# Performance work log

Hardware: AMD Instinct MI355X
Metric: run time of the kernel (lower is better)

Reference implementation:

```python
import jax, jax.numpy as jnp
import numpy as np

B, T, D, NH, F = 8, 1024, 1152, 16, 4304
HD = D // NH


def _ln(x, w, b, eps=1e-5):
    m = jnp.mean(x, axis=-1, keepdims=True)
    v = jnp.mean((x - m) ** 2, axis=-1, keepdims=True)
    return (x - m) * jax.lax.rsqrt(v + eps) * w + b


def setup_inputs() -> dict:
    key = jax.random.key(0)
    ks = jax.random.split(key, 8)
    s = 0.02
    return {
        "x": jax.random.normal(ks[0], (B, T, D), jnp.float32),
        "ln1_w": jnp.ones((D,), jnp.float32),
        "ln1_b": jnp.zeros((D,), jnp.float32),
        "wq": jax.random.normal(ks[1], (D, D), jnp.float32) * s,
        "bq": jnp.zeros((D,), jnp.float32),
        "wk": jax.random.normal(ks[2], (D, D), jnp.float32) * s,
        "bk": jnp.zeros((D,), jnp.float32),
        "wv": jax.random.normal(ks[3], (D, D), jnp.float32) * s,
        "bv": jnp.zeros((D,), jnp.float32),
        "wo": jax.random.normal(ks[4], (D, D), jnp.float32) * s,
        "bo": jnp.zeros((D,), jnp.float32),
        "ln2_w": jnp.ones((D,), jnp.float32),
        "ln2_b": jnp.zeros((D,), jnp.float32),
        "w1": jax.random.normal(ks[5], (F, D), jnp.float32) * s,
        "b1": jnp.zeros((F,), jnp.float32),
        "w2": jax.random.normal(ks[6], (D, F), jnp.float32) * s,
        "b2": jnp.zeros((D,), jnp.float32),
    }


def reference(x, ln1_w, ln1_b, wq, bq, wk, bk, wv, bv, wo, bo,
              ln2_w, ln2_b, w1, b1, w2, b2):
    b, t, d = x.shape
    h = _ln(x, ln1_w, ln1_b)
    q = h @ wq.T + bq
    k = h @ wk.T + bk
    v = h @ wv.T + bv
    # Faithful to torch: .view(B, H, T, hd) with NO transpose (non-standard split)
    q = q.reshape(b, NH, t, HD)
    k = k.reshape(b, NH, t, HD)
    v = v.reshape(b, NH, t, HD)
    scale = HD ** -0.5
    att = jnp.einsum('bhtd,bhsd->bhts', q, k) * scale  # [B,H,T,T]
    scores = jax.nn.softmax(att, axis=-1)  # dropout skipped (eval mode)
    o = jnp.einsum('bhts,bhsd->bhtd', scores, v)
    o = o.transpose(0, 2, 1, 3).reshape(b, t, d)  # transpose(1,2) + flatten(2)
    o = o @ wo.T + bo
    x1 = o + x
    h2 = _ln(x1, ln2_w, ln2_b)
    f = jax.nn.gelu(h2 @ w1.T + b1, approximate=True)
    return f @ w2.T + b2 + x1
```

## Files before the change

### kernel.cpp

```cpp
#include <hip/hip_runtime.h>
#include <cstddef>
#include <cstdint>


constexpr int kB = 8, kT = 1024, kD = 1152, kNH = 16, kF = 4304, kHD = 72;
constexpr int kNT = kB * kT;
constexpr int kFP = 4352;
constexpr int kEP = 96;
constexpr int kEV = 80;
constexpr int kFC = 2176;

typedef short bf16x8 __attribute__((ext_vector_type(8)));
typedef float f32x4 __attribute__((ext_vector_type(4)));

__device__ __forceinline__ ushort f2bf(float f) {
  union { float f; uint u; } a; a.f = f;
  const uint r = a.u + 0x7FFFu + ((a.u >> 16) & 1u);
  return (ushort)(r >> 16);
}
__device__ __forceinline__ float gelu_tanh(float x) {
  const float u = 0.7978845608028654f * (x + 0.044715f * x * x * x);
  return 0.5f * x * (1.0f + tanhf(u));
}
#define GLL16(g, s) __builtin_amdgcn_global_load_lds( \
    (const __attribute__((address_space(1))) void*)(g), \
    (__attribute__((address_space(3))) void*)(s), 16, 0, 0)

__global__ __launch_bounds__(256) void ln_kernel(const float* __restrict__ in,
                                                 const float* __restrict__ w,
                                                 const float* __restrict__ b,
                                                 ushort* __restrict__ out) {
  const int row = blockIdx.x;
  const float4* r4 = reinterpret_cast<const float4*>(in + (size_t)row * kD);
  const float4* w4 = reinterpret_cast<const float4*>(w);
  const float4* b4 = reinterpret_cast<const float4*>(b);
  const int t = threadIdx.x;
  float4 v0 = r4[t];
  float4 v1 = make_float4(0.f, 0.f, 0.f, 0.f);
  const bool second = (t < kD / 4 - 256);
  if (second) v1 = r4[t + 256];
  float s  = v0.x + v0.y + v0.z + v0.w + v1.x + v1.y + v1.z + v1.w;
  float ss = v0.x * v0.x + v0.y * v0.y + v0.z * v0.z + v0.w * v0.w +
             v1.x * v1.x + v1.y * v1.y + v1.z * v1.z + v1.w * v1.w;
  #pragma unroll
  for (int m = 1; m <= 32; m <<= 1) { s += __shfl_xor(s, m); ss += __shfl_xor(ss, m); }
  __shared__ float red[8];
  const int wave = t >> 6;
  if ((t & 63) == 0) { red[wave] = s; red[4 + wave] = ss; }
  __syncthreads();
  s  = red[0] + red[1] + red[2] + red[3];
  ss = red[4] + red[5] + red[6] + red[7];
  const float mean = s * (1.0f / kD);
  const float var  = ss * (1.0f / kD) - mean * mean;
  const float rs   = rsqrtf(var + 1e-5f);
  ushort4* o4 = reinterpret_cast<ushort4*>(out + (size_t)row * kD);
  {
    float4 W = w4[t], Bv = b4[t];
    ushort4 r;
    r.x = f2bf((v0.x - mean) * rs * W.x + Bv.x);
    r.y = f2bf((v0.y - mean) * rs * W.y + Bv.y);
    r.z = f2bf((v0.z - mean) * rs * W.z + Bv.z);
    r.w = f2bf((v0.w - mean) * rs * W.w + Bv.w);
    o4[t] = r;
  }
  if (second) {
    float4 W = w4[t + 256], Bv = b4[t + 256];
    ushort4 r;
    r.x = f2bf((v1.x - mean) * rs * W.x + Bv.x);
    r.y = f2bf((v1.y - mean) * rs * W.y + Bv.y);
    r.z = f2bf((v1.z - mean) * rs * W.z + Bv.z);
    r.w = f2bf((v1.w - mean) * rs * W.w + Bv.w);
    o4[t + 256] = r;
  }
}

__global__ __launch_bounds__(256) void cvt4_kernel(const float* __restrict__ src,
                                                   ushort* __restrict__ dst, int n4) {
  const int i = blockIdx.x * 256 + threadIdx.x;
  if (i < n4) {
    const float4 v = reinterpret_cast<const float4*>(src)[i];
    ushort4 r = { f2bf(v.x), f2bf(v.y), f2bf(v.z), f2bf(v.w) };
    reinterpret_cast<ushort4*>(dst)[i] = r;
  }
}
__global__ __launch_bounds__(256) void cvtw2_kernel(const float* __restrict__ src,
                                                    ushort* __restrict__ dst) {
  const int i = blockIdx.x * 256 + threadIdx.x;
  if (i >= kD * (kFP / 4)) return;
  const int r = i / (kFP / 4), c4 = i % (kFP / 4);
  const int c = c4 * 4;
  ushort4 o;
  if (c < kF) {
    const float4 v = *reinterpret_cast<const float4*>(src + (size_t)r * kF + c);
    o = { f2bf(v.x), f2bf(v.y), f2bf(v.z), f2bf(v.w) };
  } else o = { 0, 0, 0, 0 };
  reinterpret_cast<ushort4*>(dst + (size_t)r * kFP)[c4] = o;
}
__global__ __launch_bounds__(256) void b1pad_kernel(const float* __restrict__ src,
                                                    float* __restrict__ dst,
                                                    ushort* __restrict__ w1b) {
  const int i = blockIdx.x * 256 + threadIdx.x;
  if (i < kFP) dst[i] = (i < kF) ? src[i] : 0.f;
  const int j = i - kFP;
  if (j >= 0 && j < (kFP - kF) * kD) w1b[(size_t)kF * kD + j] = 0;
}
__global__ __launch_bounds__(256) void zfill_kernel(ushort* __restrict__ kp,
                                                    ushort* __restrict__ vt) {
  const int i = blockIdx.x * 256 + threadIdx.x;
  const int nk = 131072 * 24;
  if (i < nk) {
    const int row = i / 24, c = 72 + i % 24;
    kp[(size_t)row * kEP + c] = 0;
  } else {
    const int j = i - nk;
    if (j < 131072 * 8) {
      const int bh = j >> 13, rem = j & 8191;
      const int e = 72 + (rem >> 10), s = rem & 1023;
      vt[((size_t)bh * kEV + e) * 1024 + s] = 0;
    }
  }
}

template <int MODE, int GELU_, int BIAS_, int RES_>
__global__ __launch_bounds__(256) void gemm_mfma(
    const ushort* __restrict__ A, const ushort* __restrict__ W,
    const float* __restrict__ bias, const float* __restrict__ bias2,
    const float* __restrict__ bias3, const float* __restrict__ res,
    void* __restrict__ Cout, void* __restrict__ C2, void* __restrict__ C3,
    int M, int K, int ldw) {
  __shared__ __align__(16) ushort As[128 * 32];
  __shared__ __align__(16) ushort Bs[128 * 32];
  const int tid = threadIdx.x;
  const int l = tid & 63, w = tid >> 6;
  const int lr = l & 15, lg = l >> 4;
  const int wm = w >> 1, wn = w & 1;
  const int bn = blockIdx.x, bm = blockIdx.y;
  f32x4 acc[4][4] = {};
  const int srow = 32 * w + (l >> 2);
  const int scol = (l & 3) << 3;
  const ushort* Ag = A + (size_t)(bn * 128 + srow) * K + scol;
  const ushort* Wg = W + (size_t)(bm * 128 + srow) * ldw + scol;
  for (int k0 = 0; k0 < K; k0 += 32) {
    __syncthreads();
    #pragma unroll
    for (int i = 0; i < 2; i++) {
      GLL16(Ag + (size_t)(16 * i) * K + k0, &As[(32 * w + 16 * i) * 32]);
      GLL16(Wg + (size_t)(16 * i) * ldw + k0, &Bs[(32 * w + 16 * i) * 32]);
    }
    __syncthreads();
    bf16x8 af[4], bf[4];
    #pragma unroll
    for (int mf = 0; mf < 4; mf++)
      af[mf] = *(const bf16x8*)&As[(wm * 64 + mf * 16 + lr) * 32 + lg * 8];
    #pragma unroll
    for (int nf = 0; nf < 4; nf++)
      bf[nf] = *(const bf16x8*)&Bs[(wn * 64 + nf * 16 + lr) * 32 + lg * 8];
    #pragma unroll
    for (int mf = 0; mf < 4; mf++)
      #pragma unroll
      for (int nf = 0; nf < 4; nf++)
        acc[mf][nf] = __builtin_amdgcn_mfma_f32_16x16x32_bf16(af[mf], bf[nf], acc[mf][nf], 0, 0, 0);
  }
  if (MODE == 4) {
    const int proj = bm / 9;
    const float* bp = proj == 0 ? bias : (proj == 1 ? bias2 : bias3);
    ushort* dstp = (ushort*)(proj == 0 ? Cout : (proj == 1 ? C2 : C3));
    #pragma unroll
    for (int mf = 0; mf < 4; mf++) {
      #pragma unroll
      for (int nf = 0; nf < 4; nf++) {
        const int c = bm * 128 + wn * 64 + nf * 16 + lr;
        const int cl = c - proj * kD;
        const int jj = cl / 72, e = cl - jj * 72;
        const float bv = bp[cl];
        #pragma unroll
        for (int j = 0; j < 4; j++) {
          const int r = bn * 128 + wm * 64 + mf * 16 + lg * 4 + j;
          float v = acc[mf][nf][j] + bv;
          if (proj == 0) v *= 0.11785113019775793f;
          const int b = r >> 10, t = r & 1023;
          const int h = t >> 6, u = t & 63;
          const int s = u * 16 + jj, bh = b * 16 + h;
          const size_t dst = (proj < 2) ? ((size_t)bh * 1024 + s) * kEP + e
                                        : ((size_t)bh * kEV + e) * 1024 + s;
          dstp[dst] = f2bf(v);
        }
      }
    }
    return;
  }
  #pragma unroll
  for (int mf = 0; mf < 4; mf++) {
    #pragma unroll
    for (int nf = 0; nf < 4; nf++) {
      const int c = bm * 128 + wn * 64 + nf * 16 + lr;
      const float bv = BIAS_ ? bias[c] : 0.f;
      #pragma unroll
      for (int j = 0; j < 4; j++) {
        const int r = bn * 128 + wm * 64 + mf * 16 + lg * 4 + j;
        float v = acc[mf][nf][j] + bv;
        if (GELU_) v = gelu_tanh(v);
        if (RES_) v += res[(size_t)r * M + c];
        if (MODE == 0) ((float*)Cout)[(size_t)r * M + c] = v;
        else           ((ushort*)Cout)[(size_t)r * M + c] = f2bf(v);
      }
    }
  }
}

__global__ __launch_bounds__(256, 2) void attn_kernel(
    const ushort* __restrict__ qp, const ushort* __restrict__ kp,
    const ushort* __restrict__ vt, ushort* __restrict__ ob) {
  __shared__ __align__(16) ushort Kt[64 * 96];
  __shared__ __align__(16) ushort Vt[80 * 64];
  const int tid = threadIdx.x, l = tid & 63, w = tid >> 6;
  const int lr = l & 15, lg = l >> 4;
  const int qb = blockIdx.x, hh = blockIdx.y, bb = blockIdx.z;
  const int bh = bb * 16 + hh;
  const int s0 = qb * 256 + w * 64;
  bf16x8 qf[4][3];
  const ushort* qbase = qp + (size_t)bh * 1024 * kEP;
  #pragma unroll
  for (int qi = 0; qi < 4; qi++)
    #pragma unroll
    for (int ks = 0; ks < 3; ks++)
      qf[qi][ks] = *(const bf16x8*)(qbase + (size_t)(s0 + qi * 16 + lr) * kEP + ks * 32 + lg * 8);
  float mstate[4], lstate[4];
  #pragma unroll
  for (int i = 0; i < 4; i++) { mstate[i] = -1e30f; lstate[i] = 0.f; }
  f32x4 oacc[4][5] = {};
  const ushort* ktile0 = kp + (size_t)bh * 1024 * kEP;
  const ushort* vbase  = vt + (size_t)bh * kEV * 1024;
  const int srcA = lr + 32 * (lg & 1);
  const int srcB = srcA + 16;
  const int hi = lg >> 1;
  const int rmap = (lg << 4) + (lg << 2);

  for (int kt = 0; kt < 16; kt++) {
    __syncthreads();
    {
      const ushort* kg = ktile0 + (size_t)kt * 64 * kEP;
      #pragma unroll
      for (int i = 0; i < 3; i++) {
        const int is = w * 3 + i;
        GLL16(kg + is * 512 + l * 8, &Kt[is * 512]);
      }
    }
    {
      #pragma unroll
      for (int i = 0; i < 3; i++) {
        const int is = w + i * 4;
        if (is < 10) {
          const int e = is * 8 + (l >> 3);
          const int cg = (l & 7) ^ (e & 7);
          GLL16(vbase + (size_t)e * 1024 + kt * 64 + cg * 8, &Vt[is * 512]);
        }
      }
    }
    __syncthreads();
    f32x4 sacc[4][4];
    #pragma unroll
    for (int si = 0; si < 4; si++)
      #pragma unroll
      for (int qi = 0; qi < 4; qi++)
        sacc[si][qi] = (f32x4){0.f, 0.f, 0.f, 0.f};
    #pragma unroll
    for (int ks = 0; ks < 3; ks++) {
      bf16x8 kf[4];
      #pragma unroll
      for (int si = 0; si < 4; si++)
        kf[si] = *(const bf16x8*)&Kt[(si * 16 + lr) * 96 + ks * 32 + lg * 8];
      #pragma unroll
      for (int si = 0; si < 4; si++)
        #pragma unroll
        for (int qi = 0; qi < 4; qi++)
          sacc[si][qi] = __builtin_amdgcn_mfma_f32_16x16x32_bf16(kf[si], qf[qi][ks], sacc[si][qi], 0, 0, 0);
    }
    #pragma unroll
    for (int qi = 0; qi < 4; qi++) {
      float mx = sacc[0][qi][0];
      #pragma unroll
      for (int si = 0; si < 4; si++)
        #pragma unroll
        for (int j = 0; j < 4; j++) mx = fmaxf(mx, sacc[si][qi][j]);
      mx = fmaxf(mx, __shfl_xor(mx, 16));
      mx = fmaxf(mx, __shfl_xor(mx, 32));
      const float mo = mstate[qi], mn = fmaxf(mo, mx);
      float sum = 0.f;
      #pragma unroll
      for (int si = 0; si < 4; si++)
        #pragma unroll
        for (int j = 0; j < 4; j++) {
          const float p = __expf(sacc[si][qi][j] - mn);
          sacc[si][qi][j] = p;
          sum += p;
        }
      sum += __shfl_xor(sum, 16);
      sum += __shfl_xor(sum, 32);
      const float al = __expf(mo - mn);
      lstate[qi] = lstate[qi] * al + sum;
      mstate[qi] = mn;
      #pragma unroll
      for (int j = 0; j < 4; j++) {
        const float alj = __shfl(al, rmap + j);
        #pragma unroll
        for (int ei = 0; ei < 5; ei++) oacc[qi][ei][j] *= alj;
      }
      uint wlo[4], whi[4];
      #pragma unroll
      for (int si = 0; si < 4; si++) {
        wlo[si] = (uint)f2bf(sacc[si][qi][0]) | ((uint)f2bf(sacc[si][qi][1]) << 16);
        whi[si] = (uint)f2bf(sacc[si][qi][2]) | ((uint)f2bf(sacc[si][qi][3]) << 16);
      }
      uint A0[4], A1[4], A2[4], A3[4];
      #pragma unroll
      for (int si = 0; si < 4; si++) {
        A0[si] = (uint)__shfl((int)wlo[si], srcA);
        A1[si] = (uint)__shfl((int)whi[si], srcA);
        A2[si] = (uint)__shfl((int)wlo[si], srcB);
        A3[si] = (uint)__shfl((int)whi[si], srcB);
      }
      union U { uint u[4]; bf16x8 v; } p0, p1;
      p0.u[0] = hi ? A0[1] : A0[0];  p0.u[1] = hi ? A1[1] : A1[0];
      p0.u[2] = hi ? A2[1] : A2[0];  p0.u[3] = hi ? A3[1] : A3[0];
      p1.u[0] = hi ? A0[3] : A0[2];  p1.u[1] = hi ? A1[3] : A1[2];
      p1.u[2] = hi ? A2[3] : A2[2];  p1.u[3] = hi ? A3[3] : A3[2];
      #pragma unroll
      for (int ei = 0; ei < 5; ei++) {
        const int e = ei * 16 + lr;
        const int sw = e & 7;
        bf16x8 vb0 = *(const bf16x8*)&Vt[e * 64 + ((0 + lg) ^ sw) * 8];
        bf16x8 vb1 = *(const bf16x8*)&Vt[e * 64 + ((4 + lg) ^ sw) * 8];
        oacc[qi][ei] = __builtin_amdgcn_mfma_f32_16x16x32_bf16(p0.v, vb0, oacc[qi][ei], 0, 0, 0);
        oacc[qi][ei] = __builtin_amdgcn_mfma_f32_16x16x32_bf16(p1.v, vb1, oacc[qi][ei], 0, 0, 0);
      }
    }
  }
  #pragma unroll
  for (int qi = 0; qi < 4; qi++) {
    const float rli = 1.f / lstate[qi];
    float lij[4];
    #pragma unroll
    for (int j = 0; j < 4; j++) lij[j] = __shfl(rli, rmap + j);
    #pragma unroll
    for (int ei = 0; ei < 5; ei++) {
      const int e = ei * 16 + lr;
      if (e < 72) {
        #pragma unroll
        for (int j = 0; j < 4; j++) {
          const int s = s0 + qi * 16 + lg * 4 + j;
          ob[((size_t)bb * 1024 + s) * kD + hh * kHD + e] =
              f2bf(oacc[qi][ei][j] * lij[j]);
        }
      }
    }
  }
}

extern "C" void kernel_launch(void* const* d_in, const int* in_sizes, int n_in,
                              void* d_out, int out_size, void* d_ws, size_t ws_size,
                              hipStream_t stream) {
  const float* x    = (const float*)d_in[0];
  const float* ln1w = (const float*)d_in[1];
  const float* ln1b = (const float*)d_in[2];
  const float* wq   = (const float*)d_in[3];
  const float* bq   = (const float*)d_in[4];
  const float* wk   = (const float*)d_in[5];
  const float* bk   = (const float*)d_in[6];
  const float* wv   = (const float*)d_in[7];
  const float* bv   = (const float*)d_in[8];
  const float* wo   = (const float*)d_in[9];
  const float* bo   = (const float*)d_in[10];
  const float* ln2w = (const float*)d_in[11];
  const float* ln2b = (const float*)d_in[12];
  const float* w1   = (const float*)d_in[13];
  const float* b1   = (const float*)d_in[14];
  const float* w2   = (const float*)d_in[15];
  const float* b2   = (const float*)d_in[16];
  float* out = (float*)d_out;

  ushort* ws = (ushort*)d_ws;
  const size_t nD = (size_t)kNT * kD;
  const size_t nQK = (size_t)kB * kNH * 1024 * kEP;
  const size_t nVT = (size_t)kB * kNH * kEV * 1024;
  ushort* hb  = ws;
  ushort* qp  = hb + nD;
  ushort* kp  = qp + nQK;
  ushort* vt  = kp + nQK;
  ushort* wqb = vt + nVT;
  ushort* wkb = wqb + (size_t)kD * kD;
  ushort* wvb = wkb + (size_t)kD * kD;
  ushort* wob = wvb + (size_t)kD * kD;
  ushort* w1b = wob + (size_t)kD * kD;
  ushort* w2b = w1b + (size_t)kFP * kD;
  float*  x1  = (float*)(w2b + (size_t)kD * kFP);
  float*  b1b = x1 + nD;
  ushort* ob  = hb;
  ushort* h2b = qp;
  ushort* fb  = kp;

  const dim3 blk(256);
  const dim3 gqkv(64, 27);
  const dim3 go(64, 9);
  const dim3 gm1(64, 17);
  const dim3 ga(4, 16, 8);

  const int nDD4 = kD * kD / 4;
  cvt4_kernel<<<(nDD4 + 255) / 256, blk, 0, stream>>>(wq, wqb, nDD4);
  cvt4_kernel<<<(nDD4 + 255) / 256, blk, 0, stream>>>(wk, wkb, nDD4);
  cvt4_kernel<<<(nDD4 + 255) / 256, blk, 0, stream>>>(wv, wvb, nDD4);
  cvt4_kernel<<<(nDD4 + 255) / 256, blk, 0, stream>>>(wo, wob, nDD4);
  const int nW14 = kF * kD / 4;
  cvt4_kernel<<<(nW14 + 255) / 256, blk, 0, stream>>>(w1, w1b, nW14);
  cvtw2_kernel<<<(kD * (kFP / 4) + 255) / 256, blk, 0, stream>>>(w2, w2b);
  b1pad_kernel<<<(kFP + (kFP - kF) * kD + 255) / 256, blk, 0, stream>>>(b1, b1b, w1b);
  zfill_kernel<<<16384, blk, 0, stream>>>(kp, vt);

  ln_kernel<<<kNT, blk, 0, stream>>>(x, ln1w, ln1b, hb);
  gemm_mfma<4, 0, 1, 0><<<gqkv, blk, 0, stream>>>(hb, wqb, bq, bk, bv, nullptr,
                                                  qp, kp, vt, kD, kD, kD);
  attn_kernel<<<ga, blk, 0, stream>>>(qp, kp, vt, ob);
  gemm_mfma<0, 0, 1, 1><<<go, blk, 0, stream>>>(ob, wob, bo, nullptr, nullptr, x,
                                                x1, nullptr, nullptr, kD, kD, kD);
  ln_kernel<<<kNT, blk, 0, stream>>>(x1, ln2w, ln2b, h2b);
  gemm_mfma<1, 1, 1, 0><<<gm1, blk, 0, stream>>>(h2b, w1b, b1b, nullptr, nullptr, nullptr,
                                                 fb, nullptr, nullptr, kFC, kD, kD);
  gemm_mfma<0, 0, 1, 1><<<go, blk, 0, stream>>>(fb, w2b, b2, nullptr, nullptr, x1,
                                                out, nullptr, nullptr, kD, kFC, kFP);
  gemm_mfma<1, 1, 1, 0><<<gm1, blk, 0, stream>>>(h2b, w1b + (size_t)kFC * kD, b1b + kFC,
                                                 nullptr, nullptr, nullptr,
                                                 fb, nullptr, nullptr, kFC, kD, kD);
  gemm_mfma<0, 0, 0, 1><<<go, blk, 0, stream>>>(fb, w2b + kFC, nullptr, nullptr, nullptr,
                                                out, out, nullptr, nullptr, kD, kFC, kFP);
}
```

Before: 873.6 us.

## Replace GEMMs with 256x256-tile double-buffered MFMA kernel and unsplit FFN

Replaces the 128x128 single-buffered GEMM with a 512-thread, 256x256-tile kernel. It double-buffers LDS, loads two k-stages ahead with a swizzled layout, and raises wave priority around the MFMA block. The FFN up- and down-projections are no longer split into two halves, because the whole GELU activation now fits in the reused q/k/v workspace. The larger tiles raise data reuse and hide load latency. The cost is more LDS and registers per block, out-of-range padded tiles that read past the weights and are masked at store time, and fewer blocks for the small GEMMs.

```diff
diff --git a/kernel.cpp b/kernel.cpp
--- a/kernel.cpp
+++ b/kernel.cpp
@@ -8,7 +8,6 @@
 constexpr int kFP = 4352;
 constexpr int kEP = 96;
 constexpr int kEV = 80;
-constexpr int kFC = 2176;
 
 typedef short bf16x8 __attribute__((ext_vector_type(8)));
 typedef float f32x4 __attribute__((ext_vector_type(4)));
@@ -121,88 +120,137 @@
   }
 }
 
-template <int MODE, int GELU_, int BIAS_, int RES_>
-__global__ __launch_bounds__(256) void gemm_mfma(
+template <int MODE, int GELU_>
+__global__ __launch_bounds__(512, 2) void gemm256(
     const ushort* __restrict__ A, const ushort* __restrict__ W,
     const float* __restrict__ bias, const float* __restrict__ bias2,
     const float* __restrict__ bias3, const float* __restrict__ res,
     void* __restrict__ Cout, void* __restrict__ C2, void* __restrict__ C3,
-    int M, int K, int ldw) {
-  __shared__ __align__(16) ushort As[128 * 32];
-  __shared__ __align__(16) ushort Bs[128 * 32];
+    int Mstride, int Mreal, int K, int ldw) {
+  __shared__ __align__(16) ushort Ab[2][256 * 32];
+  __shared__ __align__(16) ushort Bb[2][256 * 32];
   const int tid = threadIdx.x;
   const int l = tid & 63, w = tid >> 6;
   const int lr = l & 15, lg = l >> 4;
-  const int wm = w >> 1, wn = w & 1;
+  const int wm = w >> 2, wn = w & 3;
   const int bn = blockIdx.x, bm = blockIdx.y;
-  f32x4 acc[4][4] = {};
-  const int srow = 32 * w + (l >> 2);
-  const int scol = (l & 3) << 3;
-  const ushort* Ag = A + (size_t)(bn * 128 + srow) * K + scol;
-  const ushort* Wg = W + (size_t)(bm * 128 + srow) * ldw + scol;
-  for (int k0 = 0; k0 < K; k0 += 32) {
-    __syncthreads();
-    #pragma unroll
-    for (int i = 0; i < 2; i++) {
-      GLL16(Ag + (size_t)(16 * i) * K + k0, &As[(32 * w + 16 * i) * 32]);
-      GLL16(Wg + (size_t)(16 * i) * ldw + k0, &Bs[(32 * w + 16 * i) * 32]);
-    }
-    __syncthreads();
-    bf16x8 af[4], bf[4];
-    #pragma unroll
-    for (int mf = 0; mf < 4; mf++)
-      af[mf] = *(const bf16x8*)&As[(wm * 64 + mf * 16 + lr) * 32 + lg * 8];
-    #pragma unroll
-    for (int nf = 0; nf < 4; nf++)
-      bf[nf] = *(const bf16x8*)&Bs[(wn * 64 + nf * 16 + lr) * 32 + lg * 8];
-    #pragma unroll
-    for (int mf = 0; mf < 4; mf++)
-      #pragma unroll
-      for (int nf = 0; nf < 4; nf++)
-        acc[mf][nf] = __builtin_amdgcn_mfma_f32_16x16x32_bf16(af[mf], bf[nf], acc[mf][nf], 0, 0, 0);
-  }
+  const int NS = K >> 5;
+
+  const int r0 = tid >> 2, c0 = (tid & 3) ^ (r0 & 3);
+  const int r1 = (512 + tid) >> 2, c1 = (tid & 3) ^ (r1 & 3);
+  const ushort* Ag0 = A + (size_t)(bn * 256 + r0) * K + c0 * 8;
+  const ushort* Ag1 = A + (size_t)(bn * 256 + r1) * K + c1 * 8;
+  const ushort* Wg0 = W + (size_t)(bm * 256 + r0) * ldw + c0 * 8;
+  const ushort* Wg1 = W + (size_t)(bm * 256 + r1) * ldw + c1 * 8;
+  const int dst0 = (w * 64) * 8;
+  const int dst1 = (512 + w * 64) * 8;
+
+  const int swz = (lg ^ (lr & 3)) * 8;
+  const int abase = (wm * 128 + lr) * 32 + swz;
+  const int bbase = (wn * 64 + lr) * 32 + swz;
+
+  f32x4 acc[8][4] = {};
+  bf16x8 A0[8], A1[8], Bf[4];
+
+  GLL16(Ag0, &Ab[0][dst0]); GLL16(Ag1, &Ab[0][dst1]);
+  GLL16(Wg0, &Bb[0][dst0]); GLL16(Wg1, &Bb[0][dst1]);
+  GLL16(Ag0 + 32, &Ab[1][dst0]); GLL16(Ag1 + 32, &Ab[1][dst1]);
+  GLL16(Wg0 + 32, &Bb[1][dst0]); GLL16(Wg1 + 32, &Bb[1][dst1]);
+  asm volatile("s_waitcnt vmcnt(4)" ::: "memory");
+  __builtin_amdgcn_s_barrier();
+  #pragma unroll
+  for (int mf = 0; mf < 8; mf++)
+    A0[mf] = *(const bf16x8*)&Ab[0][abase + mf * 512];
+  asm volatile("s_waitcnt lgkmcnt(0)" ::: "memory");
+  __builtin_amdgcn_sched_barrier(0);
+
+#define GBODY(S, AC, AA)                                                      \
+  {                                                                           \
+    asm volatile("s_waitcnt vmcnt(0)" ::: "memory");  \
+    __builtin_amdgcn_s_barrier();                                             \
+    const ushort* bb_ = &Bb[(S) & 1][0];                                      \
+    _Pragma("unroll")                                                         \
+    for (int nf = 0; nf < 4; nf++)                                            \
+      Bf[nf] = *(const bf16x8*)&bb_[bbase + nf * 512];                        \
+    __builtin_amdgcn_sched_barrier(0);        \
+    if ((S) + 1 < NS) {                                                       \
+      const ushort* ab_ = &Ab[((S) + 1) & 1][0];                              \
+      _Pragma("unroll")                                                       \
+      for (int mf = 0; mf < 8; mf++)                                          \
+        AA[mf] = *(const bf16x8*)&ab_[abase + mf * 512];                      \
+    }                                                                         \
+    asm volatile("s_waitcnt lgkmcnt(8)" ::: "memory");     \
+    __builtin_amdgcn_sched_barrier(0);                                        \
+    if ((S) + 2 < NS) {                        \
+      const int k0_ = ((S) + 2) * 32;                                         \
+      GLL16(Ag0 + k0_, &Ab[(S) & 1][dst0]);                                   \
+      GLL16(Ag1 + k0_, &Ab[(S) & 1][dst1]);                                   \
+      GLL16(Wg0 + k0_, &Bb[(S) & 1][dst0]);                                   \
+      GLL16(Wg1 + k0_, &Bb[(S) & 1][dst1]);                                   \
+    }                                                                         \
+    __builtin_amdgcn_s_setprio(1);                                            \
+    _Pragma("unroll")                                                         \
+    for (int mf = 0; mf < 8; mf++)                                            \
+      _Pragma("unroll")                                                       \
+      for (int nf = 0; nf < 4; nf++)                                          \
+        acc[mf][nf] = __builtin_amdgcn_mfma_f32_16x16x32_bf16(                \
+            AC[mf], Bf[nf], acc[mf][nf], 0, 0, 0);                            \
+    __builtin_amdgcn_s_setprio(0);                                            \
+    asm volatile("s_waitcnt lgkmcnt(0)" ::: "memory");   \
+    __builtin_amdgcn_sched_barrier(0);                                        \
+  }
+
+  for (int t = 0; t < NS / 2; t++) {
+    GBODY(2 * t, A0, A1)
+    GBODY(2 * t + 1, A1, A0)
+  }
+#undef GBODY
+
   if (MODE == 4) {
-    const int proj = bm / 9;
-    const float* bp = proj == 0 ? bias : (proj == 1 ? bias2 : bias3);
-    ushort* dstp = (ushort*)(proj == 0 ? Cout : (proj == 1 ? C2 : C3));
-    #pragma unroll
-    for (int mf = 0; mf < 4; mf++) {
-      #pragma unroll
-      for (int nf = 0; nf < 4; nf++) {
-        const int c = bm * 128 + wn * 64 + nf * 16 + lr;
-        const int cl = c - proj * kD;
-        const int jj = cl / 72, e = cl - jj * 72;
-        const float bv = bp[cl];
+    #pragma unroll
+    for (int nf = 0; nf < 4; nf++) {
+      const int c = bm * 256 + wn * 64 + nf * 16 + lr;
+      if (c >= 3 * kD) continue;
+      const int proj = c / kD;
+      const int cl = c - proj * kD;
+      const int jj = cl / 72, e = cl - jj * 72;
+      const float bv = (proj == 0 ? bias : (proj == 1 ? bias2 : bias3))[cl];
+      ushort* dp = (ushort*)(proj == 0 ? Cout : (proj == 1 ? C2 : C3));
+      #pragma unroll
+      for (int mf = 0; mf < 8; mf++) {
         #pragma unroll
         for (int j = 0; j < 4; j++) {
-          const int r = bn * 128 + wm * 64 + mf * 16 + lg * 4 + j;
+          const int r = bn * 256 + wm * 128 + mf * 16 + lg * 4 + j;
           float v = acc[mf][nf][j] + bv;
           if (proj == 0) v *= 0.11785113019775793f;
-          const int b = r >> 10, t = r & 1023;
-          const int h = t >> 6, u = t & 63;
-          const int s = u * 16 + jj, bh = b * 16 + h;
-          const size_t dst = (proj < 2) ? ((size_t)bh * 1024 + s) * kEP + e
-                                        : ((size_t)bh * kEV + e) * 1024 + s;
-          dstp[dst] = f2bf(v);
+          const int b_ = r >> 10, t_ = r & 1023;
+          const int h = t_ >> 6, u = t_ & 63;
+          const int s2 = u * 16 + jj, bh = b_ * 16 + h;
+          const size_t dst = (proj < 2) ? ((size_t)bh * 1024 + s2) * kEP + e
+                                        : ((size_t)bh * kEV + e) * 1024 + s2;
+          dp[dst] = f2bf(v);
         }
       }
     }
     return;
   }
   #pragma unroll
-  for (int mf = 0; mf < 4; mf++) {
-    #pragma unroll
-    for (int nf = 0; nf < 4; nf++) {
-      const int c = bm * 128 + wn * 64 + nf * 16 + lr;
-      const float bv = BIAS_ ? bias[c] : 0.f;
+  for (int nf = 0; nf < 4; nf++) {
+    const int c = bm * 256 + wn * 64 + nf * 16 + lr;
+    if (c >= Mreal) continue;
+    const float bv = bias[c];
+    #pragma unroll
+    for (int mf = 0; mf < 8; mf++) {
       #pragma unroll
       for (int j = 0; j < 4; j++) {
-        const int r = bn * 128 + wm * 64 + mf * 16 + lg * 4 + j;
+        const int r = bn * 256 + wm * 128 + mf * 16 + lg * 4 + j;
         float v = acc[mf][nf][j] + bv;
         if (GELU_) v = gelu_tanh(v);
-        if (RES_) v += res[(size_t)r * M + c];
-        if (MODE == 0) ((float*)Cout)[(size_t)r * M + c] = v;
-        else           ((ushort*)Cout)[(size_t)r * M + c] = f2bf(v);
+        if (MODE == 0) {
+          ((float*)Cout)[(size_t)r * Mstride + c] = v + res[(size_t)r * Mstride + c];
+        } else {
+          ((ushort*)Cout)[(size_t)r * Mstride + c] = f2bf(v);
+        }
       }
     }
   }
@@ -312,19 +360,19 @@
         wlo[si] = (uint)f2bf(sacc[si][qi][0]) | ((uint)f2bf(sacc[si][qi][1]) << 16);
         whi[si] = (uint)f2bf(sacc[si][qi][2]) | ((uint)f2bf(sacc[si][qi][3]) << 16);
       }
-      uint A0[4], A1[4], A2[4], A3[4];
+      uint Aq0[4], Aq1[4], Aq2[4], Aq3[4];
       #pragma unroll
       for (int si = 0; si < 4; si++) {
-        A0[si] = (uint)__shfl((int)wlo[si], srcA);
-        A1[si] = (uint)__shfl((int)whi[si], srcA);
-        A2[si] = (uint)__shfl((int)wlo[si], srcB);
-        A3[si] = (uint)__shfl((int)whi[si], srcB);
+        Aq0[si] = (uint)__shfl((int)wlo[si], srcA);
+        Aq1[si] = (uint)__shfl((int)whi[si], srcA);
+        Aq2[si] = (uint)__shfl((int)wlo[si], srcB);
+        Aq3[si] = (uint)__shfl((int)whi[si], srcB);
       }
       union U { uint u[4]; bf16x8 v; } p0, p1;
-      p0.u[0] = hi ? A0[1] : A0[0];  p0.u[1] = hi ? A1[1] : A1[0];
-      p0.u[2] = hi ? A2[1] : A2[0];  p0.u[3] = hi ? A3[1] : A3[0];
-      p1.u[0] = hi ? A0[3] : A0[2];  p1.u[1] = hi ? A1[3] : A1[2];
-      p1.u[2] = hi ? A2[3] : A2[2];  p1.u[3] = hi ? A3[3] : A3[2];
+      p0.u[0] = hi ? Aq0[1] : Aq0[0];  p0.u[1] = hi ? Aq1[1] : Aq1[0];
+      p0.u[2] = hi ? Aq2[1] : Aq2[0];  p0.u[3] = hi ? Aq3[1] : Aq3[0];
+      p1.u[0] = hi ? Aq0[3] : Aq0[2];  p1.u[1] = hi ? Aq1[3] : Aq1[2];
+      p1.u[2] = hi ? Aq2[3] : Aq2[2];  p1.u[3] = hi ? Aq3[3] : Aq3[2];
       #pragma unroll
       for (int ei = 0; ei < 5; ei++) {
         const int e = ei * 16 + lr;
@@ -396,13 +444,13 @@
   float*  x1  = (float*)(w2b + (size_t)kD * kFP);
   float*  b1b = x1 + nD;
   ushort* ob  = hb;
-  ushort* h2b = qp;
-  ushort* fb  = kp;
-
-  const dim3 blk(256);
-  const dim3 gqkv(64, 27);
-  const dim3 go(64, 9);
-  const dim3 gm1(64, 17);
+  ushort* h2b = hb;
+  ushort* fb  = qp;
+
+  const dim3 blk(256), blkg(512);
+  const dim3 gqkv(32, 14);
+  const dim3 go(32, 5);
+  const dim3 gw1(32, 17);
   const dim3 ga(4, 16, 8);
 
   const int nDD4 = kD * kD / 4;
@@ -417,19 +465,14 @@
   zfill_kernel<<<16384, blk, 0, stream>>>(kp, vt);
 
   ln_kernel<<<kNT, blk, 0, stream>>>(x, ln1w, ln1b, hb);
-  gemm_mfma<4, 0, 1, 0><<<gqkv, blk, 0, stream>>>(hb, wqb, bq, bk, bv, nullptr,
-                                                  qp, kp, vt, kD, kD, kD);
+  gemm256<4, 0><<<gqkv, blkg, 0, stream>>>(hb, wqb, bq, bk, bv, nullptr,
+                                           qp, kp, vt, 0, 3456, kD, kD);
   attn_kernel<<<ga, blk, 0, stream>>>(qp, kp, vt, ob);
-  gemm_mfma<0, 0, 1, 1><<<go, blk, 0, stream>>>(ob, wob, bo, nullptr, nullptr, x,
-                                                x1, nullptr, nullptr, kD, kD, kD);
+  gemm256<0, 0><<<go, blkg, 0, stream>>>(ob, wob, bo, nullptr, nullptr, x,
+                                         x1, nullptr, nullptr, kD, kD, kD, kD);
   ln_kernel<<<kNT, blk, 0, stream>>>(x1, ln2w, ln2b, h2b);
-  gemm_mfma<1, 1, 1, 0><<<gm1, blk, 0, stream>>>(h2b, w1b, b1b, nullptr, nullptr, nullptr,
-                                                 fb, nullptr, nullptr, kFC, kD, kD);
-  gemm_mfma<0, 0, 1, 1><<<go, blk, 0, stream>>>(fb, w2b, b2, nullptr, nullptr, x1,
-                                                out, nullptr, nullptr, kD, kFC, kFP);
-  gemm_mfma<1, 1, 1, 0><<<gm1, blk, 0, stream>>>(h2b, w1b + (size_t)kFC * kD, b1b + kFC,
-                                                 nullptr, nullptr, nullptr,
-                                                 fb, nullptr, nullptr, kFC, kD, kD);
-  gemm_mfma<0, 0, 0, 1><<<go, blk, 0, stream>>>(fb, w2b + kFC, nullptr, nullptr, nullptr,
-                                                out, out, nullptr, nullptr, kD, kFC, kFP);
-}
+  gemm256<1, 1><<<gw1, blkg, 0, stream>>>(h2b, w1b, b1b, nullptr, nullptr, nullptr,
+                                          fb, nullptr, nullptr, kFP, kFP, kD, kD);
+  gemm256<0, 0><<<go, blkg, 0, stream>>>(fb, w2b, b2, nullptr, nullptr, x1,
+                                         out, nullptr, nullptr, kD, kD, kFP, kFP);
+}
```

After: 790.5 us. 9.5% less time.
